# Kernel tuning notes

Hardware: AMD Instinct MI355X
Metric: run time of the kernel (lower is better)

## Reference

```python
import jax, jax.numpy as jnp
import numpy as np

G, N, E = 16, 512, 2048        # graphs, nodes/graph, edges/graph
CN, CE = 64, 64                # node / edge feature channels
K = 3                          # Laguerre polynomial order
RATIO = 0.5
KEEP = int(np.ceil(RATIO * N)) # 256 kept nodes per graph (static)
POWER_ITERS = 64               # power iteration approximating eigsh(k=1,'LM')


def setup_inputs() -> dict:
    key = jax.random.key(0)
    ks = jax.random.split(key, 10)
    x_n = jax.random.normal(ks[0], (G * N, CN), jnp.float32)
    x_e = jax.random.normal(ks[1], (G * E, CE), jnp.float32)
    # incidence endpoints per edge, local node ids, no self loops
    u = jax.random.randint(ks[2], (G, E), 0, N)
    v = (u + 1 + jax.random.randint(ks[3], (G, E), 0, N - 1)) % N
    # node-level conv graph (global ids within per-graph blocks): both directions
    offs = (jnp.arange(G) * N)[:, None]
    src_n = jnp.concatenate([(u + offs).reshape(-1), (v + offs).reshape(-1)])
    dst_n = jnp.concatenate([(v + offs).reshape(-1), (u + offs).reshape(-1)])
    edge_weight_n = jax.random.uniform(ks[4], (src_n.shape[0],), jnp.float32)
    # edge-level conv graph (global ids within per-graph edge blocks)
    ME = 4 * E
    offs_e = (jnp.arange(G) * E)[:, None]
    src_e = (jax.random.randint(ks[5], (G, ME), 0, E) + offs_e).reshape(-1)
    dst_e = (jax.random.randint(ks[6], (G, ME), 0, E) + offs_e).reshape(-1)
    edge_weight_e = jax.random.uniform(ks[7], (src_e.shape[0],), jnp.float32)
    # HodgeLaguerreConv(C -> 1, K) weights (glorot-ish) + bias (zeros init)
    W_n = jax.random.normal(ks[8], (K, CN), jnp.float32) / np.sqrt(CN)
    b_n = jnp.zeros((1,), jnp.float32)
    W_e = jax.random.normal(ks[9], (K, CE), jnp.float32) / np.sqrt(CE)
    b_e = jnp.zeros((1,), jnp.float32)
    return dict(x_n=x_n, x_e=x_e, edge_u=u, edge_v=v,
                src_n=src_n, dst_n=dst_n, edge_weight_n=edge_weight_n,
                src_e=src_e, dst_e=dst_e, edge_weight_e=edge_weight_e,
                W_n=W_n, b_n=b_n, W_e=W_e, b_e=b_e)


def hodge_laguerre(x, src, dst, w, Wk, b):
    """HodgeLaguerreConv with out_channels=1: out = sum_k T_k(L) x @ Wk[k] + b.
    T_0 = x; T_1 = x - Lx; T_{k+1} = (-L T_k + (2k+1) T_k - k T_{k-1})/(k+1)."""
    num = x.shape[0]
    def L(z):  # scatter-add message passing: out[i] = sum_{j->i} norm * z[j]
        return jax.ops.segment_sum(w[:, None] * z[src], dst, num_segments=num)
    Tx0 = x
    out = Tx0 @ Wk[0]
    Tx1 = x - L(x)
    out = out + Tx1 @ Wk[1]
    k = 1
    for i in range(2, Wk.shape[0]):
        Tx2 = (-L(Tx1) + (2 * k + 1) * Tx1 - k * Tx0) / (k + 1)
        out = out + Tx2 @ Wk[i]
        Tx0, Tx1 = Tx1, Tx2
        k += 1
    return out + b[0]


def pool_graph(sn, se, xn, xe, u, v):
    # node score augmented by |B1| @ edge_score (abs incidence gathers both endpoints)
    aug = sn.at[u].add(se).at[v].add(se)
    perm = jnp.argsort(-aug)                    # descending sort, take top KEEP
    mask_n = jnp.zeros((N,), xn.dtype).at[perm[:KEEP]].set(1.0)
    # mask_e = |B1|^T (1 - mask_n); keep edge iff both endpoints kept (== 0)
    bad = (1.0 - mask_n[u]) + (1.0 - mask_n[v])
    keep_e = (bad == 0.0).astype(xn.dtype)
    # dense incidence B1 [N, E]: -1 at source row, +1 at target row
    cols = jnp.arange(E)
    B = jnp.zeros((N, E), xn.dtype).at[u, cols].add(-1.0).at[v, cols].add(1.0)
    Bm = B * mask_n[:, None] * keep_e[None, :]  # row/col masking (zero-padded)
    L0 = Bm @ Bm.T                              # [N, N] node Laplacian
    L1 = Bm.T @ Bm                              # [E, E] edge Laplacian
    # power iteration for lambda_max(L0) (== eigsh k=1 'LM'; zero rows keep spectrum)
    w = jnp.ones((N,), xn.dtype) / np.sqrt(N)
    for _ in range(POWER_ITERS):
        w = L0 @ w
        w = w / (jnp.linalg.norm(w) + 1e-12)
    lam = w @ (L0 @ w)
    scale = 2.0 / (lam + 1e-12)
    return xn * mask_n[:, None], L0 * scale, xe * keep_e[:, None], L1 * scale


def reference(x_n, x_e, edge_u, edge_v, src_n, dst_n, edge_weight_n,
              src_e, dst_e, edge_weight_e, W_n, b_n, W_e, b_e):
    score_n = jax.nn.sigmoid(hodge_laguerre(x_n, src_n, dst_n, edge_weight_n, W_n, b_n).reshape(-1))
    score_e = jax.nn.sigmoid(hodge_laguerre(x_e, src_e, dst_e, edge_weight_e, W_e, b_e).reshape(-1))
    xn_g = (x_n * score_n[:, None]).reshape(G, N, CN)
    xe_g = (x_e * score_e[:, None]).reshape(G, E, CE)
    sn = score_n.reshape(G, N)
    se = score_e.reshape(G, E)
    return jax.vmap(pool_graph)(sn, se, xn_g, xe_g, edge_u, edge_v)
```

## Files before the change

kernel.cpp:

```cpp
#include <hip/hip_runtime.h>
#include <math.h>

#define GG 16
#define NNODE 512
#define EEDGE 2048
#define KEEPN 256
#define PITERS 64
#define NNT 8192
#define NET 32768

typedef float vfloat4 __attribute__((ext_vector_type(4)));

#define WS_C1N 0
#define WS_C2N 8192
#define WS_BN  16384
#define WS_C1E 24576
#define WS_C2E 57344
#define WS_BE  90112
#define WS_SNW 122880
#define WS_SEW 131072
#define WS_KLIST 163840
#define WS_KCNT 196608
#define WS_SCALE 196624

#define O_XN 0
#define O_L0 524288
#define O_XE 4718592
#define O_L1 6815744

#define AC_D1N 0
#define AC_D2N 8192
#define AC_E2N 16384
#define AC_D1E 24576
#define AC_D2E 57344
#define AC_E2E 90112
#define AC_TOT4 30720

#define L04 1048576
#define ZTOT4 17825792

#define DCAP 12

__global__ __launch_bounds__(512) void k_dots(
    const float* __restrict__ xn, const float* __restrict__ xe,
    const float* __restrict__ Wn, const float* __restrict__ We,
    float* __restrict__ ws, float* __restrict__ out) {
  const int tid = threadIdx.x, bid = blockIdx.x;
  if (bid >= 1024) {
    vfloat4 z = (vfloat4)(0.f);
    vfloat4* a4 = (vfloat4*)(out + O_L0);
    int base = (bid - 1024) * 512 + tid;
    #pragma unroll
    for (int k = 0; k < 4; ++k) a4[base + k * 7680] = z;
    return;
  }
  const int lane = tid & 63;
  const int wv = (bid * 512 + tid) >> 6;
  #pragma unroll
  for (int n = 0; n < 5; ++n) {
    int gw = wv + n * 8192;
    const float* x; const float* W; int row; float *c1, *c2, *bs;
    if (gw < NNT) {
      row = gw; x = xn + (size_t)row * 64; W = Wn;
      c1 = ws + WS_C1N; c2 = ws + WS_C2N; bs = ws + WS_BN;
    } else {
      row = gw - NNT;
      x = xe + (size_t)row * 64; W = We;
      c1 = ws + WS_C1E; c2 = ws + WS_C2E; bs = ws + WS_BE;
    }
    float v = x[lane];
    float r0 = v * W[lane];
    float r1 = v * W[64 + lane];
    float r2 = v * W[128 + lane];
    for (int o = 32; o; o >>= 1) {
      r0 += __shfl_xor(r0, o, 64);
      r1 += __shfl_xor(r1, o, 64);
      r2 += __shfl_xor(r2, o, 64);
    }
    if (lane == 0) { c1[row] = r1; c2[row] = r2; bs[row] = r0 + r1 + r2; }
  }
}

__global__ __launch_bounds__(512) void k_mp1(
    const int* __restrict__ src_n, const int* __restrict__ dst_n, const float* __restrict__ wn,
    const int* __restrict__ src_e, const int* __restrict__ dst_e, const float* __restrict__ we,
    const float* __restrict__ ws, float* __restrict__ out) {
  int gid = blockIdx.x * 512 + threadIdx.x;
  float* acc = (float*)(out + O_L0);
  if (gid < 65536) {
    int s = src_n[gid], d = dst_n[gid]; float w = wn[gid];
    atomicAdd(&acc[AC_D1N + d], w * ws[WS_C1N + s]);
    atomicAdd(&acc[AC_D2N + d], w * ws[WS_C2N + s]);
  } else {
    int e = gid - 65536;
    int s = src_e[e], d = dst_e[e]; float w = we[e];
    atomicAdd(&acc[AC_D1E + d], w * ws[WS_C1E + s]);
    atomicAdd(&acc[AC_D2E + d], w * ws[WS_C2E + s]);
  }
}

__global__ __launch_bounds__(512) void k_mp2(
    const int* __restrict__ src_n, const int* __restrict__ dst_n, const float* __restrict__ wn,
    const int* __restrict__ src_e, const int* __restrict__ dst_e, const float* __restrict__ we,
    float* __restrict__ ws, float* __restrict__ out) {
  int gid = blockIdx.x * 512 + threadIdx.x;
  float* acc = (float*)(out + O_L0);
  if (gid < 8192) ws[WS_C1N + gid] = 0.f;
  if (gid < 65536) {
    int s = src_n[gid], d = dst_n[gid]; float w = wn[gid];
    atomicAdd(&acc[AC_E2N + d], w * acc[AC_D2N + s]);
  } else {
    int e = gid - 65536;
    int s = src_e[e], d = dst_e[e]; float w = we[e];
    atomicAdd(&acc[AC_E2E + d], w * acc[AC_D2E + s]);
  }
}

__global__ __launch_bounds__(512) void k_score(
    const int* __restrict__ edge_u, const int* __restrict__ edge_v,
    const float* __restrict__ bnp, const float* __restrict__ bep,
    float* __restrict__ ws, float* __restrict__ out) {
  int gid = blockIdx.x * 512 + threadIdx.x;
  const float* acc = (const float*)(out + O_L0);
  if (gid < 8192) {
    int i = gid;
    float t = ws[WS_BN + i] - acc[AC_D1N + i] - 2.0f * acc[AC_D2N + i]
            + 0.5f * acc[AC_E2N + i] + bnp[0];
    float s = 1.0f / (1.0f + expf(-t));
    ws[WS_SNW + i] = s;
    atomicAdd(&ws[WS_C1N + i], s);
  } else {
    int e = gid - 8192;
    float t = ws[WS_BE + e] - acc[AC_D1E + e] - 2.0f * acc[AC_D2E + e]
            + 0.5f * acc[AC_E2E + e] + bep[0];
    float s = 1.0f / (1.0f + expf(-t));
    ws[WS_SEW + e] = s;
    int g = e >> 11;
    int u = edge_u[e], v = edge_v[e];
    atomicAdd(&ws[WS_C1N + g * NNODE + u], s);
    atomicAdd(&ws[WS_C1N + g * NNODE + v], s);
  }
}

#define PM_AUG  0
#define PM_RED  512
#define PM_IWS  520
#define PM_KCP  528
#define PM_MASK 544
#define PM_DEG  1056
#define PM_OFF  1568
#define PM_SUV  2080
#define PM_ADJ  4128
#define PM_WVA  6176
#define PM_WVB  6692
#define PM_TOT  7208
__global__ __launch_bounds__(512, 2) void k_pool(
    const int* __restrict__ edge_u, const int* __restrict__ edge_v,
    float* __restrict__ ws, float* __restrict__ out) {
  const int tid = threadIdx.x;
  if (blockIdx.x >= 16) {
    vfloat4 z = (vfloat4)(0.f);
    vfloat4* o4 = (vfloat4*)out;
    int base = (blockIdx.x - 16) * 512 + tid;
    #pragma unroll
    for (int n = 0; n < 17; ++n) {
      int i = base + n * 1048576;
      int f = (i < L04) ? (O_L0 / 4 + i) : (O_L1 / 4 + (i - L04));
      __builtin_nontemporal_store(z, &o4[f]);
    }
    return;
  }
  __shared__ float smem[PM_TOT];
  int* smi = (int*)smem;
  float* aug = smem + PM_AUG;
  float* red = smem + PM_RED;
  int* iws   = smi + PM_IWS;
  int* kcp   = smi + PM_KCP;
  int* maskS = smi + PM_MASK;
  int* degS  = smi + PM_DEG;
  int* offS  = smi + PM_OFF;
  int* suv   = smi + PM_SUV;
  unsigned short* adjU = (unsigned short*)(smi + PM_ADJ);
  float* wvA = smem + PM_WVA;
  float* wvB = smem + PM_WVB;

  const int g = blockIdx.x;
  const int roffN = g * NNODE;
  const int roffE = g * EEDGE;
  const int lane = tid & 63, wid = tid >> 6;

  float snw_r = ws[WS_SNW + roffN + tid];
  aug[tid] = ws[WS_C1N + roffN + tid];
  if (tid == 0) *kcp = 0;
  degS[tid] = 0;
  __syncthreads();

  {
    float a = aug[tid];
    int r = 0;
    #pragma unroll 8
    for (int j = 0; j < NNODE; ++j) {
      float b = aug[j];
      r += (b > a) || (b == a && j < tid);
    }
    maskS[tid] = (r < KEEPN) ? 1 : 0;
  }
  __syncthreads();
  ws[WS_SNW + roffN + tid] = snw_r * (float)maskS[tid];

  int* wsi = (int*)ws;
  {
    float seR[4]; int uR[4], vR[4];
    #pragma unroll
    for (int n = 0; n < 4; ++n) {
      int e = tid + n * 512;
      seR[n] = ws[WS_SEW + roffE + e];
      uR[n] = edge_u[roffE + e];
      vR[n] = edge_v[roffE + e];
    }
    #pragma unroll
    for (int n = 0; n < 4; ++n) {
      int e = tid + n * 512;
      int u = uR[n], v = vR[n];
      suv[e] = u | (v << 16);
      int k = maskS[u] & maskS[v];
      ws[WS_SEW + roffE + e] = seR[n] * (float)k;
      if (k) {
        int p = atomicAdd(kcp, 1);
        wsi[WS_KLIST + roffE + p] = e;
        atomicAdd(&degS[u], 1);
        atomicAdd(&degS[v], 1);
      }
    }
  }
  __syncthreads();
  if (tid == 0) wsi[WS_KCNT + g] = *kcp;

  int dv = degS[tid];
  int inc = dv;
  for (int o = 1; o < 64; o <<= 1) {
    int t = __shfl_up(inc, o, 64);
    if (lane >= o) inc += t;
  }
  if (lane == 63) iws[wid] = inc;
  __syncthreads();
  int base = 0;
  for (int k = 0; k < wid; ++k) base += iws[k];
  int myStart = base + inc - dv;
  offS[tid] = myStart;
  __syncthreads();

  for (int e = tid; e < EEDGE; e += 512) {
    int p2 = suv[e];
    int u = p2 & 0xffff, v = p2 >> 16;
    if (maskS[u] & maskS[v]) {
      int pu = atomicAdd(&offS[u], 1); adjU[pu] = (unsigned short)v;
      int pv = atomicAdd(&offS[v], 1); adjU[pv] = (unsigned short)u;
    }
  }
  __syncthreads();
  int myDeg = dv;
  int myEnd = myStart + myDeg;

  int nbr[DCAP];
  #pragma unroll
  for (int k = 0; k < DCAP; ++k)
    nbr[k] = (k < myDeg) ? (int)adjU[myStart + k] : NNODE;
  bool ovf = myDeg > DCAP;

  wvA[tid] = 0.04419417382415922f;
  if (tid == 0) { wvA[NNODE] = 0.f; wvB[NNODE] = 0.f; }
  __syncthreads();
  float* wcur = wvA; float* wnext = wvB;
  for (int it = 0; it < PITERS; ++it) {
    float tg[DCAP];
    #pragma unroll
    for (int k = 0; k < DCAP; ++k) tg[k] = wcur[nbr[k]];
    float acc = (float)myDeg * wcur[tid];
    #pragma unroll
    for (int k = 0; k < DCAP; ++k) acc -= tg[k];
    if (ovf) for (int p = myStart + DCAP; p < myEnd; ++p) acc -= wcur[(int)adjU[p]];
    if ((it & 7) == 7) {
      float sq = acc * acc;
      for (int o = 32; o; o >>= 1) sq += __shfl_xor(sq, o, 64);
      if (lane == 0) red[wid] = sq;
      __syncthreads();
      float tot = red[0] + red[1] + red[2] + red[3]
                + red[4] + red[5] + red[6] + red[7];
      wnext[tid] = acc * (1.0f / (sqrtf(tot) + 1e-12f));
    } else {
      wnext[tid] = acc;
    }
    __syncthreads();
    float* tmp = wcur; wcur = wnext; wnext = tmp;
  }
  {
    float tg[DCAP];
    #pragma unroll
    for (int k = 0; k < DCAP; ++k) tg[k] = wcur[nbr[k]];
    float wv_ = wcur[tid];
    float acc = (float)myDeg * wv_;
    #pragma unroll
    for (int k = 0; k < DCAP; ++k) acc -= tg[k];
    if (ovf) for (int p = myStart + DCAP; p < myEnd; ++p) acc -= wcur[(int)adjU[p]];
    float pr = wv_ * acc;
    for (int o = 32; o; o >>= 1) pr += __shfl_xor(pr, o, 64);
    if (lane == 0) red[wid] = pr;
    __syncthreads();
    if (tid == 0) {
      float lam = red[0] + red[1] + red[2] + red[3]
                + red[4] + red[5] + red[6] + red[7];
      ws[WS_SCALE + g] = 2.0f / (lam + 1e-12f);
    }
  }
}

__global__ __launch_bounds__(256) void k_out(
    const float* __restrict__ xn, const float* __restrict__ xe,
    const int* __restrict__ edge_u, const int* __restrict__ edge_v,
    const float* __restrict__ ws, float* __restrict__ out) {
  int b = blockIdx.x, tid = threadIdx.x;
  const int* wsi = (const int*)ws;
  if (b < 512) {
    int idx = b * 256 + tid;
    int row = idx >> 4;
    float s = ws[WS_SNW + row];
    float4 x4 = ((const float4*)xn)[idx];
    ((float4*)(out + O_XN))[idx] = make_float4(x4.x * s, x4.y * s, x4.z * s, x4.w * s);
  } else if (b < 2560) {
    int idx = (b - 512) * 256 + tid;
    int row = idx >> 4;
    float s = ws[WS_SEW + row];
    float4 x4 = ((const float4*)xe)[idx];
    ((float4*)(out + O_XE))[idx] = make_float4(x4.x * s, x4.y * s, x4.z * s, x4.w * s);
  } else if (b < 2576) {
    int g = b - 2560;
    int cnt = wsi[WS_KCNT + g];
    float s = ws[WS_SCALE + g];
    float* L0 = out + O_L0 + (long long)g * (NNODE * NNODE);
    const int* kl = wsi + WS_KLIST + g * EEDGE;
    const int* eu = edge_u + g * EEDGE;
    const int* ev = edge_v + g * EEDGE;
    for (int t = tid; t < cnt; t += 256) {
      int e = kl[t];
      int u = eu[e], v = ev[e];
      atomicAdd(&L0[u * NNODE + u], s);
      atomicAdd(&L0[v * NNODE + v], s);
      atomicAdd(&L0[u * NNODE + v], -s);
      atomicAdd(&L0[v * NNODE + u], -s);
    }
  } else {
    int q = b - 2576;
    int g = q >> 8, sb = q & 255;
    int cnt = wsi[WS_KCNT + g];
    float s = ws[WS_SCALE + g];
    float* L1 = out + O_L1 + (long long)g * (EEDGE * EEDGE);
    const int* kl = wsi + WS_KLIST + g * EEDGE;
    const int* eu = edge_u + g * EEDGE;
    const int* ev = edge_v + g * EEDGE;
    for (int a = sb; a < cnt; a += 256) {
      int e1 = kl[a];
      int u1 = eu[e1], v1 = ev[e1];
      long long rowoff = (long long)e1 * EEDGE;
      for (int b2 = tid; b2 < cnt; b2 += 256) {
        int e2 = kl[b2];
        int u2 = eu[e2], v2 = ev[e2];
        int val = (u1 == u2) + (v1 == v2) - (v1 == u2) - (u1 == v2);
        if (val) L1[rowoff + e2] = s * (float)val;
      }
    }
  }
}

extern "C" void kernel_launch(void* const* d_in, const int* in_sizes, int n_in,
                              void* d_out, int out_size, void* d_ws, size_t ws_size,
                              hipStream_t stream) {
  const float* x_n = (const float*)d_in[0];
  const float* x_e = (const float*)d_in[1];
  const int* edge_u = (const int*)d_in[2];
  const int* edge_v = (const int*)d_in[3];
  const int* src_n = (const int*)d_in[4];
  const int* dst_n = (const int*)d_in[5];
  const float* ew_n = (const float*)d_in[6];
  const int* src_e = (const int*)d_in[7];
  const int* dst_e = (const int*)d_in[8];
  const float* ew_e = (const float*)d_in[9];
  const float* W_n = (const float*)d_in[10];
  const float* b_n = (const float*)d_in[11];
  const float* W_e = (const float*)d_in[12];
  const float* b_e = (const float*)d_in[13];
  float* ws = (float*)d_ws;
  float* out = (float*)d_out;

  k_dots<<<1024 + 15, 512, 0, stream>>>(x_n, x_e, W_n, W_e, ws, out);
  k_mp1<<<384, 512, 0, stream>>>(src_n, dst_n, ew_n, src_e, dst_e, ew_e, ws, out);
  k_mp2<<<384, 512, 0, stream>>>(src_n, dst_n, ew_n, src_e, dst_e, ew_e, ws, out);
  k_score<<<80, 512, 0, stream>>>(edge_u, edge_v, b_n, b_e, ws, out);
  k_pool<<<16 + 2048, 512, 0, stream>>>(edge_u, edge_v, ws, out);
  k_out<<<6672, 256, 0, stream>>>(x_n, x_e, edge_u, edge_v, ws, out);
}
```

Measured before the change: 419.1 us.

## Replace CSR adjacency power iteration with edge-list LDS atomic scatter

```diff
diff --git a/kernel.cpp b/kernel.cpp
--- a/kernel.cpp
+++ b/kernel.cpp
@@ -34,12 +34,9 @@
 #define AC_D1E 24576
 #define AC_D2E 57344
 #define AC_E2E 90112
-#define AC_TOT4 30720
 
 #define L04 1048576
 #define ZTOT4 17825792
-
-#define DCAP 12
 
 __global__ __launch_bounds__(512) void k_dots(
     const float* __restrict__ xn, const float* __restrict__ xe,
@@ -144,16 +141,13 @@
 
 #define PM_AUG  0
 #define PM_RED  512
-#define PM_IWS  520
-#define PM_KCP  528
-#define PM_MASK 544
-#define PM_DEG  1056
-#define PM_OFF  1568
-#define PM_SUV  2080
-#define PM_ADJ  4128
-#define PM_WVA  6176
-#define PM_WVB  6692
-#define PM_TOT  7208
+#define PM_KCP  520
+#define PM_MASK 528
+#define PM_DEG  1040
+#define PM_KUV  1552
+#define PM_WVA  3600
+#define PM_WVB  4116
+#define PM_TOT  4632
 __global__ __launch_bounds__(512, 2) void k_pool(
     const int* __restrict__ edge_u, const int* __restrict__ edge_v,
     float* __restrict__ ws, float* __restrict__ out) {
@@ -174,13 +168,10 @@
   int* smi = (int*)smem;
   float* aug = smem + PM_AUG;
   float* red = smem + PM_RED;
-  int* iws   = smi + PM_IWS;
   int* kcp   = smi + PM_KCP;
   int* maskS = smi + PM_MASK;
   int* degS  = smi + PM_DEG;
-  int* offS  = smi + PM_OFF;
-  int* suv   = smi + PM_SUV;
-  unsigned short* adjU = (unsigned short*)(smi + PM_ADJ);
+  int* kuv   = smi + PM_KUV;
   float* wvA = smem + PM_WVA;
   float* wvB = smem + PM_WVB;
 
@@ -191,8 +182,16 @@
 
   float snw_r = ws[WS_SNW + roffN + tid];
   aug[tid] = ws[WS_C1N + roffN + tid];
+  degS[tid] = 0;
   if (tid == 0) *kcp = 0;
-  degS[tid] = 0;
+  float seR[4]; int uR[4], vR[4];
+  #pragma unroll
+  for (int n = 0; n < 4; ++n) {
+    int idx = roffE + tid + n * 512;
+    seR[n] = ws[WS_SEW + idx];
+    uR[n] = edge_u[idx];
+    vR[n] = edge_v[idx];
+  }
   __syncthreads();
 
   {
@@ -209,101 +208,63 @@
   ws[WS_SNW + roffN + tid] = snw_r * (float)maskS[tid];
 
   int* wsi = (int*)ws;
-  {
-    float seR[4]; int uR[4], vR[4];
-    #pragma unroll
-    for (int n = 0; n < 4; ++n) {
-      int e = tid + n * 512;
-      seR[n] = ws[WS_SEW + roffE + e];
-      uR[n] = edge_u[roffE + e];
-      vR[n] = edge_v[roffE + e];
-    }
-    #pragma unroll
-    for (int n = 0; n < 4; ++n) {
-      int e = tid + n * 512;
-      int u = uR[n], v = vR[n];
-      suv[e] = u | (v << 16);
-      int k = maskS[u] & maskS[v];
-      ws[WS_SEW + roffE + e] = seR[n] * (float)k;
-      if (k) {
-        int p = atomicAdd(kcp, 1);
-        wsi[WS_KLIST + roffE + p] = e;
-        atomicAdd(&degS[u], 1);
-        atomicAdd(&degS[v], 1);
-      }
+  #pragma unroll
+  for (int n = 0; n < 4; ++n) {
+    int e = tid + n * 512;
+    int u = uR[n], v = vR[n];
+    int k = maskS[u] & maskS[v];
+    ws[WS_SEW + roffE + e] = seR[n] * (float)k;
+    if (k) {
+      int p = atomicAdd(kcp, 1);
+      wsi[WS_KLIST + roffE + p] = e;
+      kuv[p] = u | (v << 16);
+      atomicAdd(&degS[u], 1);
+      atomicAdd(&degS[v], 1);
     }
   }
   __syncthreads();
-  if (tid == 0) wsi[WS_KCNT + g] = *kcp;
-
-  int dv = degS[tid];
-  int inc = dv;
-  for (int o = 1; o < 64; o <<= 1) {
-    int t = __shfl_up(inc, o, 64);
-    if (lane >= o) inc += t;
-  }
-  if (lane == 63) iws[wid] = inc;
-  __syncthreads();
-  int base = 0;
-  for (int k = 0; k < wid; ++k) base += iws[k];
-  int myStart = base + inc - dv;
-  offS[tid] = myStart;
-  __syncthreads();
-
-  for (int e = tid; e < EEDGE; e += 512) {
-    int p2 = suv[e];
-    int u = p2 & 0xffff, v = p2 >> 16;
-    if (maskS[u] & maskS[v]) {
-      int pu = atomicAdd(&offS[u], 1); adjU[pu] = (unsigned short)v;
-      int pv = atomicAdd(&offS[v], 1); adjU[pv] = (unsigned short)u;
-    }
-  }
-  __syncthreads();
-  int myDeg = dv;
-  int myEnd = myStart + myDeg;
-
-  int nbr[DCAP];
-  #pragma unroll
-  for (int k = 0; k < DCAP; ++k)
-    nbr[k] = (k < myDeg) ? (int)adjU[myStart + k] : NNODE;
-  bool ovf = myDeg > DCAP;
+  int cnt = *kcp;
+  if (tid == 0) wsi[WS_KCNT + g] = cnt;
+  float fdv = (float)degS[tid];
 
   wvA[tid] = 0.04419417382415922f;
-  if (tid == 0) { wvA[NNODE] = 0.f; wvB[NNODE] = 0.f; }
   __syncthreads();
   float* wcur = wvA; float* wnext = wvB;
   for (int it = 0; it < PITERS; ++it) {
-    float tg[DCAP];
-    #pragma unroll
-    for (int k = 0; k < DCAP; ++k) tg[k] = wcur[nbr[k]];
-    float acc = (float)myDeg * wcur[tid];
-    #pragma unroll
-    for (int k = 0; k < DCAP; ++k) acc -= tg[k];
-    if (ovf) for (int p = myStart + DCAP; p < myEnd; ++p) acc -= wcur[(int)adjU[p]];
+    wnext[tid] = fdv * wcur[tid];
+    __syncthreads();
+    for (int t2 = tid; t2 < cnt; t2 += 512) {
+      int uv = kuv[t2];
+      int u = uv & 0xffff, v = uv >> 16;
+      float a = wcur[v], b = wcur[u];
+      atomicAdd(&wnext[u], -a);
+      atomicAdd(&wnext[v], -b);
+    }
+    __syncthreads();
     if ((it & 7) == 7) {
-      float sq = acc * acc;
+      float a = wnext[tid];
+      float sq = a * a;
       for (int o = 32; o; o >>= 1) sq += __shfl_xor(sq, o, 64);
       if (lane == 0) red[wid] = sq;
       __syncthreads();
       float tot = red[0] + red[1] + red[2] + red[3]
                 + red[4] + red[5] + red[6] + red[7];
-      wnext[tid] = acc * (1.0f / (sqrtf(tot) + 1e-12f));
-    } else {
-      wnext[tid] = acc;
-    }
-    __syncthreads();
+      wnext[tid] = a * (1.0f / (sqrtf(tot) + 1e-12f));
+    }
     float* tmp = wcur; wcur = wnext; wnext = tmp;
   }
   {
-    float tg[DCAP];
-    #pragma unroll
-    for (int k = 0; k < DCAP; ++k) tg[k] = wcur[nbr[k]];
-    float wv_ = wcur[tid];
-    float acc = (float)myDeg * wv_;
-    #pragma unroll
-    for (int k = 0; k < DCAP; ++k) acc -= tg[k];
-    if (ovf) for (int p = myStart + DCAP; p < myEnd; ++p) acc -= wcur[(int)adjU[p]];
-    float pr = wv_ * acc;
+    wnext[tid] = fdv * wcur[tid];
+    __syncthreads();
+    for (int t2 = tid; t2 < cnt; t2 += 512) {
+      int uv = kuv[t2];
+      int u = uv & 0xffff, v = uv >> 16;
+      float a = wcur[v], b = wcur[u];
+      atomicAdd(&wnext[u], -a);
+      atomicAdd(&wnext[v], -b);
+    }
+    __syncthreads();
+    float pr = wcur[tid] * wnext[tid];
     for (int o = 32; o; o >>= 1) pr += __shfl_xor(pr, o, 64);
     if (lane == 0) red[wid] = pr;
     __syncthreads();
```

After: 526.6 us. 1.26x slower.
